# Optimization experiments

Measured on AMD Instinct MI355X. Metric: run time of the kernel, lower is better.

The kernel has to match this reference:

```python
import jax, jax.numpy as jnp
import numpy as np

NUM_JOINTS = 17

def _build_norm_adj():
    # Same skeleton as _get_skeleton_edges, made bidirectional; row-normalized
    # so that A @ x computes the per-node mean over neighbors (every joint
    # has degree >= 1, matching the original's mean aggregation branch).
    conns = [(0, 7), (7, 8), (8, 9), (9, 10), (0, 1), (1, 2), (2, 3), (0, 4),
             (4, 5), (5, 6), (8, 11), (11, 12), (12, 13), (8, 14), (14, 15), (15, 16)]
    A = np.zeros((NUM_JOINTS, NUM_JOINTS), dtype=np.float32)
    for a, b in conns:
        A[a, b] = 1.0
        A[b, a] = 1.0
    deg = A.sum(axis=1, keepdims=True)
    A = A / np.maximum(deg, 1.0)
    return jnp.asarray(A)

def _xavier(key, out_dim, in_dim):
    lim = np.sqrt(6.0 / (in_dim + out_dim)).astype(np.float32)
    return jax.random.uniform(key, (out_dim, in_dim), jnp.float32, -lim, lim)

def setup_inputs() -> dict:
    key = jax.random.key(0)
    ks = jax.random.split(key, 6)
    B, J, D_IN, H, D_OUT = 65536, NUM_JOINTS, 3, 64, 256
    x = jax.random.normal(ks[0], (B, J, D_IN), jnp.float32)
    return {
        "x": x,
        "A": _build_norm_adj(),
        "W1": _xavier(ks[1], H, D_IN), "b1": jnp.zeros((H,), jnp.float32),
        "W2": _xavier(ks[2], H, H),    "b2": jnp.zeros((H,), jnp.float32),
        "W3": _xavier(ks[3], H, H),    "b3": jnp.zeros((H,), jnp.float32),
        "Wp1": _xavier(ks[4], H, J * H), "bp1": jnp.zeros((H,), jnp.float32),
        "Wp2": _xavier(ks[5], D_OUT, H), "bp2": jnp.zeros((D_OUT,), jnp.float32),
    }

def reference(x, A, W1, b1, W2, b2, W3, b3, Wp1, bp1, Wp2, bp2):
    # GCN layer 1: neighbor-mean aggregate then linear (+ReLU; dropout = eval identity)
    h = jnp.einsum('ij,bjd->bid', A, x)            # (B, 17, 3)
    h = jax.nn.relu(h @ W1.T + b1)                 # (B, 17, 64)
    # GCN layer 2
    h = jnp.einsum('ij,bjd->bid', A, h)
    h = jax.nn.relu(h @ W2.T + b2)
    # GCN layer 3 (no activation)
    h = jnp.einsum('ij,bjd->bid', A, h)
    h = h @ W3.T + b3                              # (B, 17, 64)
    # Global pool MLP over flattened joints
    flat = h.reshape(h.shape[0], -1)               # (B, 17*64)
    z = jax.nn.relu(flat @ Wp1.T + bp1)            # (B, 64)
    return z @ Wp2.T + bp2                         # (B, 256)
```

## Files before the change

kernel.cpp:

```cpp
#include <hip/hip_runtime.h>
#include <hip/hip_bf16.h>
#include <stdint.h>

typedef __attribute__((ext_vector_type(8))) short short8;
typedef __attribute__((ext_vector_type(4))) float f32x4;
typedef __attribute__((ext_vector_type(4))) unsigned int u32x4;
typedef __attribute__((ext_vector_type(2))) unsigned int u32x2;

constexpr int kNBR[17][4] = {
    {7, 1, 4, 0}, {0, 2, 0, 0}, {1, 3, 0, 0}, {2, 0, 0, 0},
    {0, 5, 0, 0}, {4, 6, 0, 0}, {5, 0, 0, 0}, {0, 8, 0, 0},
    {7, 9, 11, 14}, {8, 10, 0, 0}, {9, 0, 0, 0}, {8, 12, 0, 0},
    {11, 13, 0, 0}, {12, 0, 0, 0}, {8, 15, 0, 0}, {14, 16, 0, 0},
    {15, 0, 0, 0}};
constexpr int kDEG[17] = {3,2,2,1,2,2,1,2,4,2,1,2,2,1,2,2,1};
constexpr float kRDEG[5] = {0.f, 1.f, 0.5f, 0.33333334f, 0.25f};
constexpr int kWNT[4] = {3, 4, 5, 5};
constexpr int kWJT[4][5] = {{8, 1, 2, 0, 0},
                            {0, 4, 5, 3, 0},
                            {7, 9, 11, 6, 10},
                            {12, 14, 15, 13, 16}};

__device__ inline unsigned short f2bf(float f) {
  union { float f; uint32_t u; } v; v.f = f;
  uint32_t u = v.u;
  uint32_t r = u + 0x7fffu + ((u >> 16) & 1u);
  return (unsigned short)(r >> 16);
}
__device__ inline uint32_t pk2(float a, float b) {
  union { __hip_bfloat162 h; uint32_t u; } v;
  v.h = __float22bfloat162_rn(make_float2(a, b));
  return v.u;
}
__device__ inline f32x4 mfma16(short8 a, short8 b, f32x4 c) {
  return __builtin_amdgcn_mfma_f32_16x16x32_bf16(a, b, c, 0, 0, 0);
}
__device__ inline int hswz(int row, int cb) {
  return row * 128 + (cb ^ ((row & 7) << 4));
}

__global__ void prep(const float* __restrict__ W1,
                     const float* __restrict__ W2,
                     const float* __restrict__ Wp2,
                     const float* __restrict__ W3,
                     const float* __restrict__ Wp1,
                     const float* __restrict__ b3,
                     const float* __restrict__ bp1,
                     const float* __restrict__ b1,
                     short* __restrict__ W1b,
                     short* __restrict__ W2b,
                     short* __restrict__ Wp2b,
                     short* __restrict__ Mb,
                     float* __restrict__ bp1p) {
  __shared__ float w3s[4096];
  __shared__ float Qs[256];
  const int tid = threadIdx.x;
  const int bx = blockIdx.x;
  if (bx < 272) {
    for (int q = tid; q < 4096; q += 256) w3s[q] = W3[q];
    {
      int ro = tid >> 6, k = tid & 63;
      int r = bx * 4 + ro;
      int f = r / 17, i = r - f * 17;
      int dj = kDEG[i];
      float s = 0.f;
#pragma unroll
      for (int t = 0; t < 4; t++) {
        if (t < dj) {
          int nb = kNBR[i][t];
          s += kRDEG[kDEG[nb]] * Wp1[f * 1088 + nb * 64 + k];
        }
      }
      Qs[ro * 64 + k] = s;
    }
    __syncthreads();
    {
      int ro = tid >> 6, c = tid & 63;
      int r = bx * 4 + ro;
      int f = r / 17, i = r - f * 17;
      float s = 0.f;
#pragma unroll
      for (int k = 0; k < 64; k++) s += Qs[ro * 64 + k] * w3s[k * 64 + c];
      int col = i * 64 + c;
      int kk = col >> 5, qq = (col >> 3) & 3, cb = col & 7;
      int w = f >> 4, l15 = f & 15;
      Mb[(((w * 34 + kk) * 64) + qq * 16 + l15) * 8 + cb] = (short)f2bf(s);
    }
  } else if (bx < 354) {
    int q = (bx - 272) * 256 + tid;
    if (q < 4096) W2b[q] = (short)f2bf(W2[q]);
    int q2 = q - 4096;
    if (q2 >= 0 && q2 < 16384) Wp2b[q2] = (short)f2bf(Wp2[q2]);
    int q3 = q - 20480;
    if (q3 >= 0 && q3 < 512) {
      int k = q3 & 7, row = q3 >> 3;
      short v = 0;
      if (k < 3) v = (short)f2bf(W1[row * 3 + k]);
      else if (k == 3) v = (short)f2bf(b1[row]);
      W1b[q3] = v;
    }
  } else {
    int wv = tid >> 6, l = tid & 63;
    int f = (bx - 354) * 4 + wv;
    float s = 0.f;
#pragma unroll
    for (int i = 0; i < 17; i++) s += Wp1[f * 1088 + i * 64 + l] * b3[l];
#pragma unroll
    for (int off = 32; off > 0; off >>= 1) s += __shfl_down(s, off);
    if (l == 0) bp1p[f] = bp1[f] + s;
  }
}

template <int WV>
__device__ __forceinline__ void waveBody(
    const short* __restrict__ Mb, const short* __restrict__ Wp2b,
    const short* __restrict__ W2b, const float* __restrict__ bp2g,
    float* __restrict__ OUT, short* hbuf, float* xs, float* sbias,
    const short8 (&w1f)[4], int bx, int lane, int ln15, int quad) {
  constexpr int NT = kWNT[WV];
  char* hb0 = (char*)hbuf;

#pragma unroll
  for (int t = 0; t < NT; t++) {
    const int j = kWJT[WV][t];
    const int dj = kDEG[j];
    const float w = kRDEG[dj];
    union { short8 s; u32x4 u; } fr[2];
#pragma unroll
    for (int g = 0; g < 2; g++) {
      const float* xsg = xs + g * 816;
      fr[g].u = (u32x4){0u, 0u, 0u, 0u};
      if (quad == 0) {
        float s0, s1, s2;
        {
          int b = ln15 * 51 + kNBR[j][0] * 3;
          s0 = xsg[b]; s1 = xsg[b + 1]; s2 = xsg[b + 2];
        }
        if (dj > 1) {
          int b = ln15 * 51 + kNBR[j][1] * 3;
          s0 += xsg[b]; s1 += xsg[b + 1]; s2 += xsg[b + 2];
        }
        if (dj > 2) {
          int b = ln15 * 51 + kNBR[j][2] * 3;
          s0 += xsg[b]; s1 += xsg[b + 1]; s2 += xsg[b + 2];
        }
        if (dj > 3) {
          int b = ln15 * 51 + kNBR[j][3] * 3;
          s0 += xsg[b]; s1 += xsg[b + 1]; s2 += xsg[b + 2];
        }
        fr[g].u.x = pk2(s0 * w, s1 * w);
        fr[g].u.y = pk2(s2 * w, 1.0f);
      }
    }
#pragma unroll
    for (int g = 0; g < 2; g++) {
      f32x4 a[4];
#pragma unroll
      for (int ft = 0; ft < 4; ft++)
        a[ft] = mfma16(w1f[ft], fr[g].s, (f32x4){0.f, 0.f, 0.f, 0.f});
#pragma unroll
      for (int ft = 0; ft < 4; ft++) {
        int fb = ft * 16 + quad * 4;
        u32x2 pk;
        pk.x = pk2(fmaxf(a[ft].x, 0.f), fmaxf(a[ft].y, 0.f));
        pk.y = pk2(fmaxf(a[ft].z, 0.f), fmaxf(a[ft].w, 0.f));
        *(u32x2*)(hb0 + g * 34816 + hswz(j * 16 + ln15, fb * 2)) = pk;
      }
    }
  }
  __syncthreads();

  short8 w2f[2][4];
#pragma unroll
  for (int kk = 0; kk < 2; kk++)
#pragma unroll
    for (int ft = 0; ft < 4; ft++)
      w2f[kk][ft] = *(const short8*)(W2b + (ft * 16 + ln15) * 64 + kk * 32 + quad * 8);

  u32x2 pkh2[2][NT][4];
#pragma unroll
  for (int t = 0; t < NT; t++) {
    const int j = kWJT[WV][t];
    const int dj = kDEG[j];
    const float w = kRDEG[dj];
#pragma unroll
    for (int g = 0; g < 2; g++) {
      f32x4 a[4];
#pragma unroll
      for (int ft = 0; ft < 4; ft++) a[ft] = (f32x4){0.f, 0.f, 0.f, 0.f};
#pragma unroll
      for (int kk = 0; kk < 2; kk++)
#pragma unroll
        for (int s = 0; s < 4; s++)
          if (s < dj) {
            const int i = kNBR[j][s];
            short8 bf = *(const short8*)(hb0 + g * 34816 +
                                         hswz(i * 16 + ln15, kk * 64 + quad * 16));
#pragma unroll
            for (int ft = 0; ft < 4; ft++)
              a[ft] = mfma16(w2f[kk][ft], bf, a[ft]);
          }
#pragma unroll
      for (int ft = 0; ft < 4; ft++) {
        int fb = ft * 16 + quad * 4;
        f32x4 bv = *(const f32x4*)&sbias[fb];
        u32x2 pk;
        pk.x = pk2(fmaxf(a[ft].x * w + bv.x, 0.f), fmaxf(a[ft].y * w + bv.y, 0.f));
        pk.y = pk2(fmaxf(a[ft].z * w + bv.z, 0.f), fmaxf(a[ft].w * w + bv.w, 0.f));
        pkh2[g][t][ft] = pk;
      }
    }
  }
  const short8* mrow = ((const short8*)Mb) + (size_t)WV * 34 * 64 + lane;
  short8 pf[8];
#pragma unroll
  for (int p = 0; p < 8; p++) pf[p] = mrow[p * 64];
  __syncthreads();

#pragma unroll
  for (int t = 0; t < NT; t++) {
    const int j = kWJT[WV][t];
#pragma unroll
    for (int g = 0; g < 2; g++)
#pragma unroll
      for (int ft = 0; ft < 4; ft++) {
        int fb = ft * 16 + quad * 4;
        *(u32x2*)(hb0 + g * 34816 + hswz(j * 16 + ln15, fb * 2)) = pkh2[g][t][ft];
      }
  }
  __syncthreads();

  const int fbw = WV * 16 + quad * 4;
  f32x4 zcv[2];
  {
    f32x4 bvp = *(const f32x4*)&sbias[64 + fbw];
    f32x4 pacc[2][4];
#pragma unroll
    for (int g = 0; g < 2; g++) {
      pacc[g][0] = bvp;
      pacc[g][1] = (f32x4){0.f, 0.f, 0.f, 0.f};
      pacc[g][2] = (f32x4){0.f, 0.f, 0.f, 0.f};
      pacc[g][3] = (f32x4){0.f, 0.f, 0.f, 0.f};
    }
#pragma unroll
    for (int kk = 0; kk < 34; kk++) {
      short8 af = pf[kk & 7];
      if (kk + 8 < 34) pf[kk & 7] = mrow[(kk + 8) * 64];
      int i = kk >> 1;
#pragma unroll
      for (int g = 0; g < 2; g++) {
        short8 bf = *(const short8*)(hb0 + g * 34816 +
                                     hswz(i * 16 + ln15, (kk & 1) * 64 + quad * 16));
        pacc[g][kk & 3] = mfma16(af, bf, pacc[g][kk & 3]);
      }
    }
    zcv[0] = (pacc[0][0] + pacc[0][1]) + (pacc[0][2] + pacc[0][3]);
    zcv[1] = (pacc[1][0] + pacc[1][1]) + (pacc[1][2] + pacc[1][3]);
  }
  short8 wp2f[4][2];
#pragma unroll
  for (int t = 0; t < 4; t++) {
    int ot = WV + 4 * t;
    wp2f[t][0] = *(const short8*)(Wp2b + (ot * 16 + ln15) * 64 + quad * 8);
    wp2f[t][1] = *(const short8*)(Wp2b + (ot * 16 + ln15) * 64 + 32 + quad * 8);
  }
#pragma unroll
  for (int g = 0; g < 2; g++) {
    char* zbB = (char*)(xs + g * 816);
    u32x2 pk;
    pk.x = pk2(fmaxf(zcv[g].x, 0.f), fmaxf(zcv[g].y, 0.f));
    pk.y = pk2(fmaxf(zcv[g].z, 0.f), fmaxf(zcv[g].w, 0.f));
    *(u32x2*)(zbB + hswz(ln15, fbw * 2)) = pk;
  }
  __syncthreads();

#pragma unroll
  for (int g = 0; g < 2; g++) {
    char* zbB = (char*)(xs + g * 816);
    short8 bf0 = *(const short8*)(zbB + hswz(ln15, quad * 16));
    short8 bf1 = *(const short8*)(zbB + hswz(ln15, 64 + quad * 16));
    int e0g = bx * 32 + g * 16;
#pragma unroll
    for (int t = 0; t < 4; t++) {
      int ot = WV + 4 * t;
      f32x4 a = (f32x4){0.f, 0.f, 0.f, 0.f};
      a = mfma16(wp2f[t][0], bf0, a);
      a = mfma16(wp2f[t][1], bf1, a);
      int ob = ot * 16 + quad * 4;
      f32x4 bv = *(const f32x4*)&bp2g[ob];
      f32x4 res = a + bv;
      *(f32x4*)(OUT + (size_t)(e0g + ln15) * 256 + ob) = res;
    }
  }
}

__launch_bounds__(256, 2)
__global__ void gcn_main(const float* __restrict__ X,
                         const short* __restrict__ Mb,
                         const short* __restrict__ Wp2b,
                         const short* __restrict__ W2b,
                         const short* __restrict__ W1b,
                         const float* __restrict__ bp1p,
                         const float* __restrict__ b2g,
                         const float* __restrict__ bp2g,
                         float* __restrict__ OUT) {
  __shared__ __align__(16) short hbuf[2 * 272 * 64];
  __shared__ __align__(16) float xs[2 * 816];
  __shared__ __align__(16) float sbias[128];

  const int tid = threadIdx.x;
  const int wave = tid >> 6;
  const int lane = tid & 63;
  const int ln15 = lane & 15;
  const int quad = lane >> 4;
  const int bx = blockIdx.x;

  for (int q = tid; q < 408; q += 256)
    ((f32x4*)xs)[q] = ((const f32x4*)(X + (size_t)bx * 1632))[q];
  short8 w1f[4];
#pragma unroll
  for (int ft = 0; ft < 4; ft++)
    w1f[ft] = *(const short8*)(W1b + (ft * 16 + ln15) * 8);
  if (tid < 128) {
    sbias[tid] = (tid < 64) ? b2g[tid] : bp1p[tid - 64];
  }
  __syncthreads();

  if (wave == 0)
    waveBody<0>(Mb, Wp2b, W2b, bp2g, OUT, hbuf, xs, sbias, w1f, bx, lane, ln15, quad);
  else if (wave == 1)
    waveBody<1>(Mb, Wp2b, W2b, bp2g, OUT, hbuf, xs, sbias, w1f, bx, lane, ln15, quad);
  else if (wave == 2)
    waveBody<2>(Mb, Wp2b, W2b, bp2g, OUT, hbuf, xs, sbias, w1f, bx, lane, ln15, quad);
  else
    waveBody<3>(Mb, Wp2b, W2b, bp2g, OUT, hbuf, xs, sbias, w1f, bx, lane, ln15, quad);
}

extern "C" void kernel_launch(void* const* d_in, const int* in_sizes, int n_in,
                              void* d_out, int out_size, void* d_ws, size_t ws_size,
                              hipStream_t stream) {
  const float* X = (const float*)d_in[0];
  const float* W1 = (const float*)d_in[2];
  const float* b1 = (const float*)d_in[3];
  const float* W2 = (const float*)d_in[4];
  const float* b2 = (const float*)d_in[5];
  const float* W3 = (const float*)d_in[6];
  const float* b3 = (const float*)d_in[7];
  const float* Wp1 = (const float*)d_in[8];
  const float* bp1 = (const float*)d_in[9];
  const float* Wp2 = (const float*)d_in[10];
  const float* bp2 = (const float*)d_in[11];
  float* OUT = (float*)d_out;
  const int B = in_sizes[0] / 51;

  char* ws = (char*)d_ws;
  short* Mb = (short*)(ws + 0);
  short* Wp2b = (short*)(ws + 139264);
  short* W2b = (short*)(ws + 172032);
  short* W1b = (short*)(ws + 180224);
  float* bp1p = (float*)(ws + 181248);

  prep<<<370, 256, 0, stream>>>(W1, W2, Wp2, W3, Wp1, b3, bp1, b1,
                                W1b, W2b, Wp2b, Mb, bp1p);
  gcn_main<<<B / 32, 256, 0, stream>>>(X, Mb, Wp2b, W2b, W1b, bp1p,
                                       b2, bp2, OUT);
}
```

Baseline: 155.2 us.

## Restructure to single-wave blocks processing 16 samples each without barriers

Replaces the 4-wave, 32-sample block (joints split across waves, synchronised with __syncthreads) with a single 64-lane wave per block handling 16 samples and all 17 joints, so no block barriers are needed. Each wave now computes all four pooled-feature tiles and all 16 output tiles, with a deeper prefetch of the pooled-layer weights and more register state (pkh2[17][4], wp2f[16][2], pf[24]). This removes cross-wave synchronisation and load imbalance, at the cost of high register pressure that may limit occupancy, and every wave now re-reads the full Wp1 and Wp2 weights.

Result: slower. 188.3 us (+21.3%).

```diff
diff --git a/kernel.cpp b/kernel.cpp
--- a/kernel.cpp
+++ b/kernel.cpp
@@ -15,11 +15,6 @@
     {15, 0, 0, 0}};
 constexpr int kDEG[17] = {3,2,2,1,2,2,1,2,4,2,1,2,2,1,2,2,1};
 constexpr float kRDEG[5] = {0.f, 1.f, 0.5f, 0.33333334f, 0.25f};
-constexpr int kWNT[4] = {3, 4, 5, 5};
-constexpr int kWJT[4][5] = {{8, 1, 2, 0, 0},
-                            {0, 4, 5, 3, 0},
-                            {7, 9, 11, 6, 10},
-                            {12, 14, 15, 13, 16}};
 
 __device__ inline unsigned short f2bf(float f) {
   union { float f; uint32_t u; } v; v.f = f;
@@ -111,190 +106,7 @@
   }
 }
 
-template <int WV>
-__device__ __forceinline__ void waveBody(
-    const short* __restrict__ Mb, const short* __restrict__ Wp2b,
-    const short* __restrict__ W2b, const float* __restrict__ bp2g,
-    float* __restrict__ OUT, short* hbuf, float* xs, float* sbias,
-    const short8 (&w1f)[4], int bx, int lane, int ln15, int quad) {
-  constexpr int NT = kWNT[WV];
-  char* hb0 = (char*)hbuf;
-
-#pragma unroll
-  for (int t = 0; t < NT; t++) {
-    const int j = kWJT[WV][t];
-    const int dj = kDEG[j];
-    const float w = kRDEG[dj];
-    union { short8 s; u32x4 u; } fr[2];
-#pragma unroll
-    for (int g = 0; g < 2; g++) {
-      const float* xsg = xs + g * 816;
-      fr[g].u = (u32x4){0u, 0u, 0u, 0u};
-      if (quad == 0) {
-        float s0, s1, s2;
-        {
-          int b = ln15 * 51 + kNBR[j][0] * 3;
-          s0 = xsg[b]; s1 = xsg[b + 1]; s2 = xsg[b + 2];
-        }
-        if (dj > 1) {
-          int b = ln15 * 51 + kNBR[j][1] * 3;
-          s0 += xsg[b]; s1 += xsg[b + 1]; s2 += xsg[b + 2];
-        }
-        if (dj > 2) {
-          int b = ln15 * 51 + kNBR[j][2] * 3;
-          s0 += xsg[b]; s1 += xsg[b + 1]; s2 += xsg[b + 2];
-        }
-        if (dj > 3) {
-          int b = ln15 * 51 + kNBR[j][3] * 3;
-          s0 += xsg[b]; s1 += xsg[b + 1]; s2 += xsg[b + 2];
-        }
-        fr[g].u.x = pk2(s0 * w, s1 * w);
-        fr[g].u.y = pk2(s2 * w, 1.0f);
-      }
-    }
-#pragma unroll
-    for (int g = 0; g < 2; g++) {
-      f32x4 a[4];
-#pragma unroll
-      for (int ft = 0; ft < 4; ft++)
-        a[ft] = mfma16(w1f[ft], fr[g].s, (f32x4){0.f, 0.f, 0.f, 0.f});
-#pragma unroll
-      for (int ft = 0; ft < 4; ft++) {
-        int fb = ft * 16 + quad * 4;
-        u32x2 pk;
-        pk.x = pk2(fmaxf(a[ft].x, 0.f), fmaxf(a[ft].y, 0.f));
-        pk.y = pk2(fmaxf(a[ft].z, 0.f), fmaxf(a[ft].w, 0.f));
-        *(u32x2*)(hb0 + g * 34816 + hswz(j * 16 + ln15, fb * 2)) = pk;
-      }
-    }
-  }
-  __syncthreads();
-
-  short8 w2f[2][4];
-#pragma unroll
-  for (int kk = 0; kk < 2; kk++)
-#pragma unroll
-    for (int ft = 0; ft < 4; ft++)
-      w2f[kk][ft] = *(const short8*)(W2b + (ft * 16 + ln15) * 64 + kk * 32 + quad * 8);
-
-  u32x2 pkh2[2][NT][4];
-#pragma unroll
-  for (int t = 0; t < NT; t++) {
-    const int j = kWJT[WV][t];
-    const int dj = kDEG[j];
-    const float w = kRDEG[dj];
-#pragma unroll
-    for (int g = 0; g < 2; g++) {
-      f32x4 a[4];
-#pragma unroll
-      for (int ft = 0; ft < 4; ft++) a[ft] = (f32x4){0.f, 0.f, 0.f, 0.f};
-#pragma unroll
-      for (int kk = 0; kk < 2; kk++)
-#pragma unroll
-        for (int s = 0; s < 4; s++)
-          if (s < dj) {
-            const int i = kNBR[j][s];
-            short8 bf = *(const short8*)(hb0 + g * 34816 +
-                                         hswz(i * 16 + ln15, kk * 64 + quad * 16));
-#pragma unroll
-            for (int ft = 0; ft < 4; ft++)
-              a[ft] = mfma16(w2f[kk][ft], bf, a[ft]);
-          }
-#pragma unroll
-      for (int ft = 0; ft < 4; ft++) {
-        int fb = ft * 16 + quad * 4;
-        f32x4 bv = *(const f32x4*)&sbias[fb];
-        u32x2 pk;
-        pk.x = pk2(fmaxf(a[ft].x * w + bv.x, 0.f), fmaxf(a[ft].y * w + bv.y, 0.f));
-        pk.y = pk2(fmaxf(a[ft].z * w + bv.z, 0.f), fmaxf(a[ft].w * w + bv.w, 0.f));
-        pkh2[g][t][ft] = pk;
-      }
-    }
-  }
-  const short8* mrow = ((const short8*)Mb) + (size_t)WV * 34 * 64 + lane;
-  short8 pf[8];
-#pragma unroll
-  for (int p = 0; p < 8; p++) pf[p] = mrow[p * 64];
-  __syncthreads();
-
-#pragma unroll
-  for (int t = 0; t < NT; t++) {
-    const int j = kWJT[WV][t];
-#pragma unroll
-    for (int g = 0; g < 2; g++)
-#pragma unroll
-      for (int ft = 0; ft < 4; ft++) {
-        int fb = ft * 16 + quad * 4;
-        *(u32x2*)(hb0 + g * 34816 + hswz(j * 16 + ln15, fb * 2)) = pkh2[g][t][ft];
-      }
-  }
-  __syncthreads();
-
-  const int fbw = WV * 16 + quad * 4;
-  f32x4 zcv[2];
-  {
-    f32x4 bvp = *(const f32x4*)&sbias[64 + fbw];
-    f32x4 pacc[2][4];
-#pragma unroll
-    for (int g = 0; g < 2; g++) {
-      pacc[g][0] = bvp;
-      pacc[g][1] = (f32x4){0.f, 0.f, 0.f, 0.f};
-      pacc[g][2] = (f32x4){0.f, 0.f, 0.f, 0.f};
-      pacc[g][3] = (f32x4){0.f, 0.f, 0.f, 0.f};
-    }
-#pragma unroll
-    for (int kk = 0; kk < 34; kk++) {
-      short8 af = pf[kk & 7];
-      if (kk + 8 < 34) pf[kk & 7] = mrow[(kk + 8) * 64];
-      int i = kk >> 1;
-#pragma unroll
-      for (int g = 0; g < 2; g++) {
-        short8 bf = *(const short8*)(hb0 + g * 34816 +
-                                     hswz(i * 16 + ln15, (kk & 1) * 64 + quad * 16));
-        pacc[g][kk & 3] = mfma16(af, bf, pacc[g][kk & 3]);
-      }
-    }
-    zcv[0] = (pacc[0][0] + pacc[0][1]) + (pacc[0][2] + pacc[0][3]);
-    zcv[1] = (pacc[1][0] + pacc[1][1]) + (pacc[1][2] + pacc[1][3]);
-  }
-  short8 wp2f[4][2];
-#pragma unroll
-  for (int t = 0; t < 4; t++) {
-    int ot = WV + 4 * t;
-    wp2f[t][0] = *(const short8*)(Wp2b + (ot * 16 + ln15) * 64 + quad * 8);
-    wp2f[t][1] = *(const short8*)(Wp2b + (ot * 16 + ln15) * 64 + 32 + quad * 8);
-  }
-#pragma unroll
-  for (int g = 0; g < 2; g++) {
-    char* zbB = (char*)(xs + g * 816);
-    u32x2 pk;
-    pk.x = pk2(fmaxf(zcv[g].x, 0.f), fmaxf(zcv[g].y, 0.f));
-    pk.y = pk2(fmaxf(zcv[g].z, 0.f), fmaxf(zcv[g].w, 0.f));
-    *(u32x2*)(zbB + hswz(ln15, fbw * 2)) = pk;
-  }
-  __syncthreads();
-
-#pragma unroll
-  for (int g = 0; g < 2; g++) {
-    char* zbB = (char*)(xs + g * 816);
-    short8 bf0 = *(const short8*)(zbB + hswz(ln15, quad * 16));
-    short8 bf1 = *(const short8*)(zbB + hswz(ln15, 64 + quad * 16));
-    int e0g = bx * 32 + g * 16;
-#pragma unroll
-    for (int t = 0; t < 4; t++) {
-      int ot = WV + 4 * t;
-      f32x4 a = (f32x4){0.f, 0.f, 0.f, 0.f};
-      a = mfma16(wp2f[t][0], bf0, a);
-      a = mfma16(wp2f[t][1], bf1, a);
-      int ob = ot * 16 + quad * 4;
-      f32x4 bv = *(const f32x4*)&bp2g[ob];
-      f32x4 res = a + bv;
-      *(f32x4*)(OUT + (size_t)(e0g + ln15) * 256 + ob) = res;
-    }
-  }
-}
-
-__launch_bounds__(256, 2)
+__launch_bounds__(64, 1)
 __global__ void gcn_main(const float* __restrict__ X,
                          const short* __restrict__ Mb,
                          const short* __restrict__ Wp2b,
@@ -304,36 +116,173 @@
                          const float* __restrict__ b2g,
                          const float* __restrict__ bp2g,
                          float* __restrict__ OUT) {
-  __shared__ __align__(16) short hbuf[2 * 272 * 64];
-  __shared__ __align__(16) float xs[2 * 816];
-  __shared__ __align__(16) float sbias[128];
-
-  const int tid = threadIdx.x;
-  const int wave = tid >> 6;
-  const int lane = tid & 63;
+  __shared__ __align__(16) short hbuf[17408];
+  __shared__ __align__(16) float xs[816];
+  const int lane = threadIdx.x;
   const int ln15 = lane & 15;
   const int quad = lane >> 4;
-  const int bx = blockIdx.x;
-
-  for (int q = tid; q < 408; q += 256)
-    ((f32x4*)xs)[q] = ((const f32x4*)(X + (size_t)bx * 1632))[q];
+  const int e0 = blockIdx.x * 16;
+  char* hb = (char*)hbuf;
+
+  {
+    const f32x4* src = (const f32x4*)(X + (size_t)e0 * 51);
+    f32x4* dst = (f32x4*)xs;
+    dst[lane] = src[lane];
+    dst[lane + 64] = src[lane + 64];
+    dst[lane + 128] = src[lane + 128];
+    if (lane < 12) dst[lane + 192] = src[lane + 192];
+  }
   short8 w1f[4];
 #pragma unroll
   for (int ft = 0; ft < 4; ft++)
     w1f[ft] = *(const short8*)(W1b + (ft * 16 + ln15) * 8);
-  if (tid < 128) {
-    sbias[tid] = (tid < 64) ? b2g[tid] : bp1p[tid - 64];
-  }
-  __syncthreads();
-
-  if (wave == 0)
-    waveBody<0>(Mb, Wp2b, W2b, bp2g, OUT, hbuf, xs, sbias, w1f, bx, lane, ln15, quad);
-  else if (wave == 1)
-    waveBody<1>(Mb, Wp2b, W2b, bp2g, OUT, hbuf, xs, sbias, w1f, bx, lane, ln15, quad);
-  else if (wave == 2)
-    waveBody<2>(Mb, Wp2b, W2b, bp2g, OUT, hbuf, xs, sbias, w1f, bx, lane, ln15, quad);
-  else
-    waveBody<3>(Mb, Wp2b, W2b, bp2g, OUT, hbuf, xs, sbias, w1f, bx, lane, ln15, quad);
+  short8 w2f[2][4];
+#pragma unroll
+  for (int kk = 0; kk < 2; kk++)
+#pragma unroll
+    for (int ft = 0; ft < 4; ft++)
+      w2f[kk][ft] = *(const short8*)(W2b + (ft * 16 + ln15) * 64 + kk * 32 + quad * 8);
+  f32x4 bv2[4];
+#pragma unroll
+  for (int ft = 0; ft < 4; ft++)
+    bv2[ft] = *(const f32x4*)(b2g + ft * 16 + quad * 4);
+
+#pragma unroll
+  for (int j = 0; j < 17; j++) {
+    const int dj = kDEG[j];
+    const float w = kRDEG[dj];
+    union { short8 s; u32x4 u; } fr;
+    fr.u = (u32x4){0u, 0u, 0u, 0u};
+    if (quad == 0) {
+      float s0, s1, s2;
+      {
+        int b = ln15 * 51 + kNBR[j][0] * 3;
+        s0 = xs[b]; s1 = xs[b + 1]; s2 = xs[b + 2];
+      }
+      if (dj > 1) {
+        int b = ln15 * 51 + kNBR[j][1] * 3;
+        s0 += xs[b]; s1 += xs[b + 1]; s2 += xs[b + 2];
+      }
+      if (dj > 2) {
+        int b = ln15 * 51 + kNBR[j][2] * 3;
+        s0 += xs[b]; s1 += xs[b + 1]; s2 += xs[b + 2];
+      }
+      if (dj > 3) {
+        int b = ln15 * 51 + kNBR[j][3] * 3;
+        s0 += xs[b]; s1 += xs[b + 1]; s2 += xs[b + 2];
+      }
+      fr.u.x = pk2(s0 * w, s1 * w);
+      fr.u.y = pk2(s2 * w, 1.0f);
+    }
+    f32x4 a[4];
+#pragma unroll
+    for (int ft = 0; ft < 4; ft++)
+      a[ft] = mfma16(w1f[ft], fr.s, (f32x4){0.f, 0.f, 0.f, 0.f});
+#pragma unroll
+    for (int ft = 0; ft < 4; ft++) {
+      int fb = ft * 16 + quad * 4;
+      u32x2 pk;
+      pk.x = pk2(fmaxf(a[ft].x, 0.f), fmaxf(a[ft].y, 0.f));
+      pk.y = pk2(fmaxf(a[ft].z, 0.f), fmaxf(a[ft].w, 0.f));
+      *(u32x2*)(hb + hswz(j * 16 + ln15, fb * 2)) = pk;
+    }
+  }
+
+  u32x2 pkh2[17][4];
+#pragma unroll
+  for (int j = 0; j < 17; j++) {
+    f32x4 a[4];
+#pragma unroll
+    for (int ft = 0; ft < 4; ft++) a[ft] = (f32x4){0.f, 0.f, 0.f, 0.f};
+#pragma unroll
+    for (int s = 0; s < 4; s++)
+      if (s < kDEG[j]) {
+        const int i = kNBR[j][s];
+#pragma unroll
+        for (int kk = 0; kk < 2; kk++) {
+          short8 bf = *(const short8*)(hb + hswz(i * 16 + ln15, kk * 64 + quad * 16));
+#pragma unroll
+          for (int ft = 0; ft < 4; ft++)
+            a[ft] = mfma16(w2f[kk][ft], bf, a[ft]);
+        }
+      }
+    const float w = kRDEG[kDEG[j]];
+#pragma unroll
+    for (int ft = 0; ft < 4; ft++) {
+      u32x2 pk;
+      pk.x = pk2(fmaxf(a[ft].x * w + bv2[ft].x, 0.f),
+                 fmaxf(a[ft].y * w + bv2[ft].y, 0.f));
+      pk.y = pk2(fmaxf(a[ft].z * w + bv2[ft].z, 0.f),
+                 fmaxf(a[ft].w * w + bv2[ft].w, 0.f));
+      pkh2[j][ft] = pk;
+    }
+  }
+
+  const short8* mrow = ((const short8*)Mb) + lane;
+  short8 pf[24];
+#pragma unroll
+  for (int k5 = 0; k5 < 6; k5++)
+#pragma unroll
+    for (int w4 = 0; w4 < 4; w4++)
+      pf[k5 * 4 + w4] = mrow[(w4 * 34 + k5) * 64];
+
+#pragma unroll
+  for (int j = 0; j < 17; j++)
+#pragma unroll
+    for (int ft = 0; ft < 4; ft++) {
+      int fb = ft * 16 + quad * 4;
+      *(u32x2*)(hb + hswz(j * 16 + ln15, fb * 2)) = pkh2[j][ft];
+    }
+
+  f32x4 pacc[4][2];
+#pragma unroll
+  for (int w4 = 0; w4 < 4; w4++) {
+    pacc[w4][0] = *(const f32x4*)(bp1p + w4 * 16 + quad * 4);
+    pacc[w4][1] = (f32x4){0.f, 0.f, 0.f, 0.f};
+  }
+#pragma unroll
+  for (int kk = 0; kk < 34; kk++) {
+    const int i = kk >> 1;
+    short8 bf = *(const short8*)(hb + hswz(i * 16 + ln15, (kk & 1) * 64 + quad * 16));
+#pragma unroll
+    for (int w4 = 0; w4 < 4; w4++) {
+      short8 af = pf[(4 * kk + w4) % 24];
+      if (kk + 6 < 34) pf[(4 * kk + w4) % 24] = mrow[(w4 * 34 + kk + 6) * 64];
+      pacc[w4][kk & 1] = mfma16(af, bf, pacc[w4][kk & 1]);
+    }
+  }
+  f32x4 zcv[4];
+#pragma unroll
+  for (int w4 = 0; w4 < 4; w4++) zcv[w4] = pacc[w4][0] + pacc[w4][1];
+
+  short8 wp2f[16][2];
+#pragma unroll
+  for (int t = 0; t < 16; t++) {
+    wp2f[t][0] = *(const short8*)(Wp2b + (t * 16 + ln15) * 64 + quad * 8);
+    wp2f[t][1] = *(const short8*)(Wp2b + (t * 16 + ln15) * 64 + 32 + quad * 8);
+  }
+  char* zbB = (char*)xs;
+#pragma unroll
+  for (int w4 = 0; w4 < 4; w4++) {
+    int fb = w4 * 16 + quad * 4;
+    u32x2 pk;
+    pk.x = pk2(fmaxf(zcv[w4].x, 0.f), fmaxf(zcv[w4].y, 0.f));
+    pk.y = pk2(fmaxf(zcv[w4].z, 0.f), fmaxf(zcv[w4].w, 0.f));
+    *(u32x2*)(zbB + hswz(ln15, fb * 2)) = pk;
+  }
+
+  short8 bf0 = *(const short8*)(zbB + hswz(ln15, quad * 16));
+  short8 bf1 = *(const short8*)(zbB + hswz(ln15, 64 + quad * 16));
+#pragma unroll
+  for (int t = 0; t < 16; t++) {
+    f32x4 a = (f32x4){0.f, 0.f, 0.f, 0.f};
+    a = mfma16(wp2f[t][0], bf0, a);
+    a = mfma16(wp2f[t][1], bf1, a);
+    int ob = t * 16 + quad * 4;
+    f32x4 bv = *(const f32x4*)&bp2g[ob];
+    f32x4 res = a + bv;
+    *(f32x4*)(OUT + (size_t)(e0 + ln15) * 256 + ob) = res;
+  }
 }
 
 extern "C" void kernel_launch(void* const* d_in, const int* in_sizes, int n_in,
@@ -362,6 +311,6 @@
 
   prep<<<370, 256, 0, stream>>>(W1, W2, Wp2, W3, Wp1, b3, bp1, b1,
                                 W1b, W2b, Wp2b, Mb, bp1p);
-  gcn_main<<<B / 32, 256, 0, stream>>>(X, Mb, Wp2b, W2b, W1b, bp1p,
-                                       b2, bp2, OUT);
-}
+  gcn_main<<<B / 16, 64, 0, stream>>>(X, Mb, Wp2b, W2b, W1b, bp1p,
+                                      b2, bp2, OUT);
+}
```

## Compute pool layer from register-resident layer-2 outputs with split-K reduction

Applied to the files above, without the earlier changes.

Each wave now multiplies its own joints' layer-2 activations, still held in registers, against all four output-feature tiles of the fused W3·Wp1 matrix. The partial results are reduced across waves through shared memory. Before, every wave wrote its activations to shared memory, synchronized, and re-read all 17 joints for one feature tile. The precomputed matrix layout is rearranged so its K ordering matches the register fragment layout, which removes the LDS round-trip of the hidden state. The cost is a four-way cross-wave reduction in shared memory, more accumulators per wave, and an extra barrier.

New measurement: 148.6 us. -4.3%, faster.

```diff
diff --git a/kernel.cpp b/kernel.cpp
--- a/kernel.cpp
+++ b/kernel.cpp
@@ -81,10 +81,12 @@
       float s = 0.f;
 #pragma unroll
       for (int k = 0; k < 64; k++) s += Qs[ro * 64 + k] * w3s[k * 64 + c];
-      int col = i * 64 + c;
-      int kk = col >> 5, qq = (col >> 3) & 3, cb = col & 7;
+      int h = c >> 5;
+      int c5 = c & 31;
+      int q = (c5 >> 2) & 3;
+      int m = ((c5 >> 4) << 2) | (c5 & 3);
       int w = f >> 4, l15 = f & 15;
-      Mb[(((w * 34 + kk) * 64) + qq * 16 + l15) * 8 + cb] = (short)f2bf(s);
+      Mb[((((w * 17 + i) * 2 + h) * 64) + q * 16 + l15) * 8 + m] = (short)f2bf(s);
     }
   } else if (bx < 354) {
     int q = (bx - 272) * 256 + tid;
@@ -113,7 +115,7 @@
 
 template <int WV>
 __device__ __forceinline__ void waveBody(
-    const short* __restrict__ Mb, const short* __restrict__ Wp2b,
+    const short* __restrict__ Mb2, const short* __restrict__ Wp2b,
     const short* __restrict__ W2b, const float* __restrict__ bp2g,
     float* __restrict__ OUT, short* hbuf, float* xs, float* sbias,
     const short8 (&w1f)[4], int bx, int lane, int ln15, int quad) {
@@ -189,17 +191,18 @@
 #pragma unroll
       for (int ft = 0; ft < 4; ft++) a[ft] = (f32x4){0.f, 0.f, 0.f, 0.f};
 #pragma unroll
-      for (int kk = 0; kk < 2; kk++)
-#pragma unroll
-        for (int s = 0; s < 4; s++)
-          if (s < dj) {
-            const int i = kNBR[j][s];
+      for (int s = 0; s < 4; s++)
+        if (s < dj) {
+          const int i = kNBR[j][s];
+#pragma unroll
+          for (int kk = 0; kk < 2; kk++) {
             short8 bf = *(const short8*)(hb0 + g * 34816 +
                                          hswz(i * 16 + ln15, kk * 64 + quad * 16));
 #pragma unroll
             for (int ft = 0; ft < 4; ft++)
               a[ft] = mfma16(w2f[kk][ft], bf, a[ft]);
           }
+        }
 #pragma unroll
       for (int ft = 0; ft < 4; ft++) {
         int fb = ft * 16 + quad * 4;
@@ -211,52 +214,40 @@
       }
     }
   }
-  const short8* mrow = ((const short8*)Mb) + (size_t)WV * 34 * 64 + lane;
-  short8 pf[8];
-#pragma unroll
-  for (int p = 0; p < 8; p++) pf[p] = mrow[p * 64];
-  __syncthreads();
-
+
+  f32x4 zacc[4][2];
+#pragma unroll
+  for (int w4 = 0; w4 < 4; w4++) {
+    zacc[w4][0] = (f32x4){0.f, 0.f, 0.f, 0.f};
+    zacc[w4][1] = (f32x4){0.f, 0.f, 0.f, 0.f};
+  }
+  const short8* mb = (const short8*)Mb2;
 #pragma unroll
   for (int t = 0; t < NT; t++) {
-    const int j = kWJT[WV][t];
+    const int i = kWJT[WV][t];
+#pragma unroll
+    for (int h = 0; h < 2; h++) {
+      union { short8 s; u32x4 u; } bf0, bf1;
+      bf0.u = (u32x4){pkh2[0][t][2 * h].x, pkh2[0][t][2 * h].y,
+                      pkh2[0][t][2 * h + 1].x, pkh2[0][t][2 * h + 1].y};
+      bf1.u = (u32x4){pkh2[1][t][2 * h].x, pkh2[1][t][2 * h].y,
+                      pkh2[1][t][2 * h + 1].x, pkh2[1][t][2 * h + 1].y};
+#pragma unroll
+      for (int w4 = 0; w4 < 4; w4++) {
+        short8 af = mb[(((w4 * 17 + i) * 2 + h) * 64) + lane];
+        zacc[w4][0] = mfma16(af, bf0.s, zacc[w4][0]);
+        zacc[w4][1] = mfma16(af, bf1.s, zacc[w4][1]);
+      }
+    }
+  }
+  __syncthreads();
+
+#pragma unroll
+  for (int w4 = 0; w4 < 4; w4++)
 #pragma unroll
     for (int g = 0; g < 2; g++)
-#pragma unroll
-      for (int ft = 0; ft < 4; ft++) {
-        int fb = ft * 16 + quad * 4;
-        *(u32x2*)(hb0 + g * 34816 + hswz(j * 16 + ln15, fb * 2)) = pkh2[g][t][ft];
-      }
-  }
-  __syncthreads();
-
-  const int fbw = WV * 16 + quad * 4;
-  f32x4 zcv[2];
-  {
-    f32x4 bvp = *(const f32x4*)&sbias[64 + fbw];
-    f32x4 pacc[2][4];
-#pragma unroll
-    for (int g = 0; g < 2; g++) {
-      pacc[g][0] = bvp;
-      pacc[g][1] = (f32x4){0.f, 0.f, 0.f, 0.f};
-      pacc[g][2] = (f32x4){0.f, 0.f, 0.f, 0.f};
-      pacc[g][3] = (f32x4){0.f, 0.f, 0.f, 0.f};
-    }
-#pragma unroll
-    for (int kk = 0; kk < 34; kk++) {
-      short8 af = pf[kk & 7];
-      if (kk + 8 < 34) pf[kk & 7] = mrow[(kk + 8) * 64];
-      int i = kk >> 1;
-#pragma unroll
-      for (int g = 0; g < 2; g++) {
-        short8 bf = *(const short8*)(hb0 + g * 34816 +
-                                     hswz(i * 16 + ln15, (kk & 1) * 64 + quad * 16));
-        pacc[g][kk & 3] = mfma16(af, bf, pacc[g][kk & 3]);
-      }
-    }
-    zcv[0] = (pacc[0][0] + pacc[0][1]) + (pacc[0][2] + pacc[0][3]);
-    zcv[1] = (pacc[1][0] + pacc[1][1]) + (pacc[1][2] + pacc[1][3]);
-  }
+      *(f32x4*)(hb0 + WV * 8192 + (w4 * 2 + g) * 1024 + lane * 16) = zacc[w4][g];
+
   short8 wp2f[4][2];
 #pragma unroll
   for (int t = 0; t < 4; t++) {
@@ -264,27 +255,40 @@
     wp2f[t][0] = *(const short8*)(Wp2b + (ot * 16 + ln15) * 64 + quad * 8);
     wp2f[t][1] = *(const short8*)(Wp2b + (ot * 16 + ln15) * 64 + 32 + quad * 8);
   }
+  __syncthreads();
+
+  char* zbB = (char*)xs;
+#pragma unroll
+  for (int half = 0; half < 2; half++) {
+    const int gw = WV + half * 4;
+    const int g = gw & 1, w4 = gw >> 1;
+    f32x4 s0 = *(const f32x4*)(hb0 + 0 * 8192 + gw * 1024 + lane * 16);
+    f32x4 s1 = *(const f32x4*)(hb0 + 1 * 8192 + gw * 1024 + lane * 16);
+    f32x4 s2 = *(const f32x4*)(hb0 + 2 * 8192 + gw * 1024 + lane * 16);
+    f32x4 s3 = *(const f32x4*)(hb0 + 3 * 8192 + gw * 1024 + lane * 16);
+    f32x4 s = (s0 + s1) + (s2 + s3);
+    const int e = lane & 15, qd = lane >> 4;
+    const int f0 = w4 * 16 + qd * 4;
+    f32x4 bv = *(const f32x4*)&sbias[64 + f0];
+    u32x2 pk;
+    pk.x = pk2(fmaxf(s.x + bv.x, 0.f), fmaxf(s.y + bv.y, 0.f));
+    pk.y = pk2(fmaxf(s.z + bv.z, 0.f), fmaxf(s.w + bv.w, 0.f));
+    *(u32x2*)(zbB + g * 2048 + e * 128 + ((f0 * 2) ^ ((e & 7) << 4))) = pk;
+  }
+  __syncthreads();
+
+  const int e0 = bx * 32;
 #pragma unroll
   for (int g = 0; g < 2; g++) {
-    char* zbB = (char*)(xs + g * 816);
-    u32x2 pk;
-    pk.x = pk2(fmaxf(zcv[g].x, 0.f), fmaxf(zcv[g].y, 0.f));
-    pk.y = pk2(fmaxf(zcv[g].z, 0.f), fmaxf(zcv[g].w, 0.f));
-    *(u32x2*)(zbB + hswz(ln15, fbw * 2)) = pk;
-  }
-  __syncthreads();
-
-#pragma unroll
-  for (int g = 0; g < 2; g++) {
-    char* zbB = (char*)(xs + g * 816);
-    short8 bf0 = *(const short8*)(zbB + hswz(ln15, quad * 16));
-    short8 bf1 = *(const short8*)(zbB + hswz(ln15, 64 + quad * 16));
-    int e0g = bx * 32 + g * 16;
+    short8 bf0 = *(const short8*)(zbB + g * 2048 + ln15 * 128 +
+                                  ((quad * 16) ^ ((ln15 & 7) << 4)));
+    short8 bf1 = *(const short8*)(zbB + g * 2048 + ln15 * 128 +
+                                  ((64 + quad * 16) ^ ((ln15 & 7) << 4)));
+    int e0g = e0 + g * 16;
 #pragma unroll
     for (int t = 0; t < 4; t++) {
       int ot = WV + 4 * t;
-      f32x4 a = (f32x4){0.f, 0.f, 0.f, 0.f};
-      a = mfma16(wp2f[t][0], bf0, a);
+      f32x4 a = mfma16(wp2f[t][0], bf0, (f32x4){0.f, 0.f, 0.f, 0.f});
       a = mfma16(wp2f[t][1], bf1, a);
       int ob = ot * 16 + quad * 4;
       f32x4 bv = *(const f32x4*)&bp2g[ob];
@@ -296,7 +300,7 @@
 
 __launch_bounds__(256, 2)
 __global__ void gcn_main(const float* __restrict__ X,
-                         const short* __restrict__ Mb,
+                         const short* __restrict__ Mb2,
                          const short* __restrict__ Wp2b,
                          const short* __restrict__ W2b,
                          const short* __restrict__ W1b,
@@ -321,19 +325,17 @@
 #pragma unroll
   for (int ft = 0; ft < 4; ft++)
     w1f[ft] = *(const short8*)(W1b + (ft * 16 + ln15) * 8);
-  if (tid < 128) {
-    sbias[tid] = (tid < 64) ? b2g[tid] : bp1p[tid - 64];
-  }
+  if (tid < 128) sbias[tid] = (tid < 64) ? b2g[tid] : bp1p[tid - 64];
   __syncthreads();
 
   if (wave == 0)
-    waveBody<0>(Mb, Wp2b, W2b, bp2g, OUT, hbuf, xs, sbias, w1f, bx, lane, ln15, quad);
+    waveBody<0>(Mb2, Wp2b, W2b, bp2g, OUT, hbuf, xs, sbias, w1f, bx, lane, ln15, quad);
   else if (wave == 1)
-    waveBody<1>(Mb, Wp2b, W2b, bp2g, OUT, hbuf, xs, sbias, w1f, bx, lane, ln15, quad);
+    waveBody<1>(Mb2, Wp2b, W2b, bp2g, OUT, hbuf, xs, sbias, w1f, bx, lane, ln15, quad);
   else if (wave == 2)
-    waveBody<2>(Mb, Wp2b, W2b, bp2g, OUT, hbuf, xs, sbias, w1f, bx, lane, ln15, quad);
+    waveBody<2>(Mb2, Wp2b, W2b, bp2g, OUT, hbuf, xs, sbias, w1f, bx, lane, ln15, quad);
   else
-    waveBody<3>(Mb, Wp2b, W2b, bp2g, OUT, hbuf, xs, sbias, w1f, bx, lane, ln15, quad);
+    waveBody<3>(Mb2, Wp2b, W2b, bp2g, OUT, hbuf, xs, sbias, w1f, bx, lane, ln15, quad);
 }
 
 extern "C" void kernel_launch(void* const* d_in, const int* in_sizes, int n_in,
```
